# Kernel tuning notes

Hardware: AMD Instinct MI355X
Metric: run time of the kernel (lower is better)

The kernel has to match this reference:

```python
import jax, jax.numpy as jnp
import numpy as np

N = 100000   # nodes
E = 1600000  # edges
IN, H, C = 128, 128, 64
LN_EPS = 1e-5


def _xavier(key, fan_in, fan_out):
    lim = jnp.sqrt(6.0 / (fan_in + fan_out)).astype(jnp.float32)
    return jax.random.uniform(key, (fan_in, fan_out), jnp.float32, -lim, lim)


def setup_inputs() -> dict:
    key = jax.random.key(0)
    ks = jax.random.split(key, 6)
    feats = jax.random.normal(ks[0], (N, IN), jnp.float32)
    src = jax.random.randint(ks[1], (E,), 0, N, jnp.int32)
    dst = jax.random.randint(ks[2], (E,), 0, N, jnp.int32)
    return {
        "feats": feats, "src": src, "dst": dst,
        "W0": _xavier(ks[3], IN, H), "b0": jnp.zeros((H,), jnp.float32),
        "g0": jnp.ones((H,), jnp.float32), "be0": jnp.zeros((H,), jnp.float32),
        "W1": _xavier(ks[4], H, H), "b1": jnp.zeros((H,), jnp.float32),
        "g1": jnp.ones((H,), jnp.float32), "be1": jnp.zeros((H,), jnp.float32),
        "W2": _xavier(ks[5], H, C), "b2": jnp.zeros((C,), jnp.float32),
    }


def _gcn_agg(h, src, dst):
    # symmetric GCN normalization: out[v] = sum_{(u,v) in E} h[u] / sqrt(deg_out(u) * deg_in(v))
    ones = jnp.ones(src.shape, jnp.float32)
    deg_out = jax.ops.segment_sum(ones, src, num_segments=N)
    deg_in = jax.ops.segment_sum(ones, dst, num_segments=N)
    norm_o = jax.lax.rsqrt(jnp.maximum(deg_out, 1.0))
    norm_i = jax.lax.rsqrt(jnp.maximum(deg_in, 1.0))
    msg = (h * norm_o[:, None])[src]                       # [E, d] gather
    agg = jax.ops.segment_sum(msg, dst, num_segments=N)    # [N, d] scatter-add
    return agg * norm_i[:, None]


def _layernorm(x, gamma, beta):
    mu = jnp.mean(x, axis=-1, keepdims=True)
    var = jnp.mean(jnp.square(x - mu), axis=-1, keepdims=True)
    return (x - mu) * jax.lax.rsqrt(var + LN_EPS) * gamma + beta


def reference(feats, src, dst, W0, b0, g0, be0, W1, b1, g1, be1, W2, b2):
    # layer 0: agg -> matmul -> bias -> dropout(eval: identity) -> layernorm -> relu
    h = _gcn_agg(feats, src, dst) @ W0 + b0
    h = jax.nn.relu(_layernorm(h, g0, be0))
    # layer 1
    h = _gcn_agg(h, src, dst) @ W1 + b1
    h = jax.nn.relu(_layernorm(h, g1, be1))
    # final layer: agg -> matmul -> bias
    out = _gcn_agg(h, src, dst) @ W2 + b2
    return out
```

## Files before the change

### kernel.cpp

```cpp
#include <hip/hip_runtime.h>

constexpr float LN_EPS = 1e-5f;

typedef __bf16 bf16x8 __attribute__((ext_vector_type(8)));
typedef float f32x4 __attribute__((ext_vector_type(4)));

__device__ __forceinline__ unsigned short f2bf(float f) {
  unsigned int u = __float_as_uint(f);
  u = (u + 0x7fffu + ((u >> 16) & 1u)) >> 16;
  return (unsigned short)u;
}
__device__ __forceinline__ unsigned int pk2(float x, float y) {
  return (unsigned int)f2bf(x) | ((unsigned int)f2bf(y) << 16);
}
__device__ __forceinline__ float bflo(unsigned int p) { return __uint_as_float(p << 16); }
__device__ __forceinline__ float bfhi(unsigned int p) { return __uint_as_float(p & 0xffff0000u); }

#define NPB 256
#define CHUNK 4096

__global__ __launch_bounds__(256) void passA_kernel(
    const int* __restrict__ src, const int* __restrict__ dst,
    int* __restrict__ cntD, int* __restrict__ cntS, int NB, int NBLK, int E) {
  extern __shared__ int sh[];
  for (int j = threadIdx.x; j < 2 * NB; j += 256) sh[j] = 0;
  __syncthreads();
  const int blk = blockIdx.x;
  const int base = blk * CHUNK;
  const int end = min(base + CHUNK, E);
  for (int i = base + threadIdx.x; i < end; i += 256) {
    atomicAdd(&sh[dst[i] >> 8], 1);
    atomicAdd(&sh[NB + (src[i] >> 8)], 1);
  }
  __syncthreads();
  for (int j = threadIdx.x; j < NB; j += 256) {
    cntD[j * NBLK + blk] = sh[j];
    cntS[j * NBLK + blk] = sh[NB + j];
  }
}

__global__ __launch_bounds__(512) void scan1_kernel(
    const int* __restrict__ cntD, const int* __restrict__ cntS,
    int* __restrict__ offLD, int* __restrict__ offLS,
    int* __restrict__ totD, int* __restrict__ totS, int NB, int NBLK) {
  __shared__ int p[512];
  const int t = threadIdx.x;
  const bool isS = blockIdx.x >= NB;
  const int b = isS ? blockIdx.x - NB : blockIdx.x;
  const int* cnt = isS ? cntS : cntD;
  int* offL = isS ? offLS : offLD;
  int own = (t < NBLK) ? cnt[b * NBLK + t] : 0;
  p[t] = own;
  __syncthreads();
  for (int off = 1; off < 512; off <<= 1) {
    int x = (t >= off) ? p[t - off] : 0;
    __syncthreads();
    p[t] += x;
    __syncthreads();
  }
  if (t < NBLK) offL[b * NBLK + t] = p[t] - own;
  if (t == 511) (isS ? totS : totD)[b] = p[511];
}

__global__ __launch_bounds__(512) void scan2_kernel(
    const int* __restrict__ totD, const int* __restrict__ totS,
    int* __restrict__ bktD, int* __restrict__ bktS,
    int* __restrict__ row_st, int NB, int N, int E) {
  __shared__ int p[512];
  const int t = threadIdx.x;
  int own = (t < NB) ? totD[t] : 0;
  p[t] = own;
  __syncthreads();
  for (int off = 1; off < 512; off <<= 1) {
    int x = (t >= off) ? p[t - off] : 0;
    __syncthreads();
    p[t] += x;
    __syncthreads();
  }
  if (t < NB) bktD[t] = p[t] - own;
  __syncthreads();
  int own2 = (t < NB) ? totS[t] : 0;
  p[t] = own2;
  __syncthreads();
  for (int off = 1; off < 512; off <<= 1) {
    int x = (t >= off) ? p[t - off] : 0;
    __syncthreads();
    p[t] += x;
    __syncthreads();
  }
  if (t < NB) bktS[t] = p[t] - own2;
  if (t == 0) {
    bktD[NB] = E;
    bktS[NB] = E;
    row_st[N] = E;
  }
}

__global__ __launch_bounds__(256) void passB_kernel(
    const int* __restrict__ src, const int* __restrict__ dst,
    const int* __restrict__ offLD, const int* __restrict__ offLS,
    const int* __restrict__ bkt_stD, const int* __restrict__ bkt_stS,
    unsigned int* __restrict__ packedD, unsigned char* __restrict__ srcS,
    int NB, int NBLK, int E) {
  __shared__ unsigned int sD[CHUNK];
  __shared__ unsigned short bD_[CHUNK];
  __shared__ unsigned char sS_[CHUNK];
  __shared__ unsigned short bS_[CHUNK];
  __shared__ int hD[512], lD[512], hS[512], lS[512];
  const int t = threadIdx.x;
  const int blk = blockIdx.x;
  const int base = blk * CHUNK;
  const int end = min(base + CHUNK, E);
  const int cnt = end - base;
  hD[t] = 0; hD[t + 256] = 0; hS[t] = 0; hS[t + 256] = 0;
  __syncthreads();
  for (int i = base + t; i < end; i += 256) {
    atomicAdd(&hD[dst[i] >> 8], 1);
    atomicAdd(&hS[src[i] >> 8], 1);
  }
  __syncthreads();
  int oD0 = hD[t], oD1 = hD[t + 256], oS0 = hS[t], oS1 = hS[t + 256];
  for (int off = 1; off < 512; off <<= 1) {
    int xd0 = (t >= off) ? hD[t - off] : 0;
    int xd1 = (t + 256 >= off) ? hD[t + 256 - off] : 0;
    int xs0 = (t >= off) ? hS[t - off] : 0;
    int xs1 = (t + 256 >= off) ? hS[t + 256 - off] : 0;
    __syncthreads();
    hD[t] += xd0; hD[t + 256] += xd1;
    hS[t] += xs0; hS[t + 256] += xs1;
    __syncthreads();
  }
  lD[t] = hD[t] - oD0; lD[t + 256] = hD[t + 256] - oD1;
  lS[t] = hS[t] - oS0; lS[t + 256] = hS[t + 256] - oS1;
  __syncthreads();
  hD[t] = lD[t]; hD[t + 256] = lD[t + 256];
  hS[t] = lS[t]; hS[t + 256] = lS[t + 256];
  __syncthreads();
  for (int i = base + t; i < end; i += 256) {
    const int d = dst[i];
    const int s = src[i];
    const int bD = d >> 8;
    const int pD = atomicAdd(&hD[bD], 1);
    sD[pD] = ((unsigned int)(d & 255) << 24) | (unsigned int)s;
    bD_[pD] = (unsigned short)bD;
    const int bS = s >> 8;
    const int pS = atomicAdd(&hS[bS], 1);
    sS_[pS] = (unsigned char)(s & 255);
    bS_[pS] = (unsigned short)bS;
  }
  __syncthreads();
  for (int i = t; i < cnt; i += 256) {
    const int bD = bD_[i];
    packedD[bkt_stD[bD] + offLD[bD * NBLK + blk] + (i - lD[bD])] = sD[i];
    const int bS = bS_[i];
    srcS[bkt_stS[bS] + offLS[bS * NBLK + blk] + (i - lS[bS])] = sS_[i];
  }
}

__global__ __launch_bounds__(256) void passC_kernel(
    const unsigned int* __restrict__ packed, const int* __restrict__ bucket_start,
    int* __restrict__ row_st, float* __restrict__ ni,
    int* __restrict__ edge_src, int N) {
  __shared__ int cnt[NPB];
  __shared__ int cur[NPB];
  __shared__ int tmp[NPB];
  const int b = blockIdx.x;
  const int t = threadIdx.x;
  const int v0 = b * NPB;
  const int bs = bucket_start[b];
  const int be = bucket_start[b + 1];
  cnt[t] = 0;
  __syncthreads();
  for (int i = bs + t; i < be; i += 256)
    atomicAdd(&cnt[packed[i] >> 24], 1);
  __syncthreads();
  int own = cnt[t];
  tmp[t] = own;
  __syncthreads();
  for (int off = 1; off < NPB; off <<= 1) {
    int x = (t >= off) ? tmp[t - off] : 0;
    __syncthreads();
    tmp[t] += x;
    __syncthreads();
  }
  const int pref = tmp[t] - own;
  if (v0 + t < N) {
    row_st[v0 + t] = bs + pref;
    ni[v0 + t] = rsqrtf(fmaxf((float)own, 1.0f));
  }
  cur[t] = bs + pref;
  __syncthreads();
  for (int i = bs + t; i < be; i += 256) {
    unsigned int p = packed[i];
    int pos = atomicAdd(&cur[p >> 24], 1);
    edge_src[pos] = (int)(p & 0xFFFFFFu);
  }
}

__global__ __launch_bounds__(256) void passD_kernel(
    const unsigned char* __restrict__ srcS, const int* __restrict__ bkt_stS,
    float* __restrict__ no, int N) {
  __shared__ int cnt[NPB];
  const int b = blockIdx.x;
  const int t = threadIdx.x;
  cnt[t] = 0;
  __syncthreads();
  const int bs = bkt_stS[b];
  const int be = bkt_stS[b + 1];
  for (int i = bs + t; i < be; i += 256)
    atomicAdd(&cnt[srcS[i]], 1);
  __syncthreads();
  const int v = b * NPB + t;
  if (v < N) no[v] = rsqrtf(fmaxf((float)cnt[t], 1.0f));
}

__global__ void wconv_kernel(const float* __restrict__ W, unsigned short* __restrict__ Wt,
                             int K, int C) {
  int i = blockIdx.x * blockDim.x + threadIdx.x;
  if (i < K * C) {
    int k = i / C, c = i - k * C;
    Wt[c * K + k] = f2bf(W[i]);
  }
}

__global__ __launch_bounds__(256) void featconv_kernel(const float* __restrict__ F,
                                                       const float* __restrict__ no,
                                                       unsigned short* __restrict__ out, int N) {
  int row = blockIdx.x * 8 + (threadIdx.x >> 5);
  if (row >= N) return;
  int c = (threadIdx.x & 31) * 4;
  float4 v = *reinterpret_cast<const float4*>(F + (size_t)row * 128 + c);
  float nof = no[row];
  uint2 p = {pk2(v.x * nof, v.y * nof), pk2(v.z * nof, v.w * nof)};
  *reinterpret_cast<uint2*>(out + (size_t)row * 128 + c) = p;
}

__global__ __launch_bounds__(256) void gather_agg_b(
    const unsigned short* __restrict__ hB, const int* __restrict__ row_start,
    const int* __restrict__ edge_src, const float* __restrict__ ni,
    unsigned short* __restrict__ aggB, int N) {
  const int v = blockIdx.x * 4 + (threadIdx.x >> 6);
  if (v >= N) return;
  const int l = threadIdx.x & 63;
  const int half = l >> 5;
  const int lane = l & 31;
  const int s = row_start[v];
  const int e = row_start[v + 1];
  const int co = 4 * lane;
  float a0 = 0, a1 = 0, a2 = 0, a3 = 0;
  float b0 = 0, b1 = 0, b2 = 0, b3 = 0;
  float c0 = 0, c1 = 0, c2 = 0, c3 = 0;
  float d0 = 0, d1 = 0, d2 = 0, d3 = 0;
  int j = s;
  for (; j + 8 <= e; j += 8) {
    int u0 = edge_src[j + half];
    int u1 = edge_src[j + 2 + half];
    int u2 = edge_src[j + 4 + half];
    int u3 = edge_src[j + 6 + half];
    uint2 p0 = *reinterpret_cast<const uint2*>(hB + (size_t)u0 * 128 + co);
    uint2 p1 = *reinterpret_cast<const uint2*>(hB + (size_t)u1 * 128 + co);
    uint2 p2 = *reinterpret_cast<const uint2*>(hB + (size_t)u2 * 128 + co);
    uint2 p3 = *reinterpret_cast<const uint2*>(hB + (size_t)u3 * 128 + co);
    a0 += bflo(p0.x); a1 += bfhi(p0.x); a2 += bflo(p0.y); a3 += bfhi(p0.y);
    b0 += bflo(p1.x); b1 += bfhi(p1.x); b2 += bflo(p1.y); b3 += bfhi(p1.y);
    c0 += bflo(p2.x); c1 += bfhi(p2.x); c2 += bflo(p2.y); c3 += bfhi(p2.y);
    d0 += bflo(p3.x); d1 += bfhi(p3.x); d2 += bflo(p3.y); d3 += bfhi(p3.y);
  }
  for (; j + 2 <= e; j += 2) {
    int u0 = edge_src[j + half];
    uint2 p0 = *reinterpret_cast<const uint2*>(hB + (size_t)u0 * 128 + co);
    a0 += bflo(p0.x); a1 += bfhi(p0.x); a2 += bflo(p0.y); a3 += bfhi(p0.y);
  }
  if (j < e && half == 0) {
    int u0 = edge_src[j];
    uint2 p0 = *reinterpret_cast<const uint2*>(hB + (size_t)u0 * 128 + co);
    a0 += bflo(p0.x); a1 += bfhi(p0.x); a2 += bflo(p0.y); a3 += bfhi(p0.y);
  }
  a0 = (a0 + b0) + (c0 + d0);
  a1 = (a1 + b1) + (c1 + d1);
  a2 = (a2 + b2) + (c2 + d2);
  a3 = (a3 + b3) + (c3 + d3);
  a0 += __shfl_xor(a0, 32);
  a1 += __shfl_xor(a1, 32);
  a2 += __shfl_xor(a2, 32);
  a3 += __shfl_xor(a3, 32);
  if (half == 0) {
    const float niv = ni[v];
    uint2 po = {pk2(a0 * niv, a1 * niv), pk2(a2 * niv, a3 * niv)};
    *reinterpret_cast<uint2*>(aggB + (size_t)v * 128 + co) = po;
  }
}

__global__ __launch_bounds__(256) void gather_out(
    const unsigned short* __restrict__ zB, const int* __restrict__ row_start,
    const int* __restrict__ edge_src, const float* __restrict__ ni,
    const float* __restrict__ bias, float* __restrict__ out, int N) {
  const int v = blockIdx.x * 4 + (threadIdx.x >> 6);
  if (v >= N) return;
  const int l = threadIdx.x & 63;
  const int half = l >> 5;
  const int lane = l & 31;
  const int s = row_start[v];
  const int e = row_start[v + 1];
  const int co = 2 * lane;
  float a0 = 0, a1 = 0, b0 = 0, b1 = 0, c0 = 0, c1 = 0, d0 = 0, d1 = 0;
  int j = s;
  for (; j + 8 <= e; j += 8) {
    int u0 = edge_src[j + half];
    int u1 = edge_src[j + 2 + half];
    int u2 = edge_src[j + 4 + half];
    int u3 = edge_src[j + 6 + half];
    unsigned int p0 = *reinterpret_cast<const unsigned int*>(zB + (size_t)u0 * 64 + co);
    unsigned int p1 = *reinterpret_cast<const unsigned int*>(zB + (size_t)u1 * 64 + co);
    unsigned int p2 = *reinterpret_cast<const unsigned int*>(zB + (size_t)u2 * 64 + co);
    unsigned int p3 = *reinterpret_cast<const unsigned int*>(zB + (size_t)u3 * 64 + co);
    a0 += bflo(p0); a1 += bfhi(p0);
    b0 += bflo(p1); b1 += bfhi(p1);
    c0 += bflo(p2); c1 += bfhi(p2);
    d0 += bflo(p3); d1 += bfhi(p3);
  }
  for (; j + 2 <= e; j += 2) {
    int u0 = edge_src[j + half];
    unsigned int p0 = *reinterpret_cast<const unsigned int*>(zB + (size_t)u0 * 64 + co);
    a0 += bflo(p0); a1 += bfhi(p0);
  }
  if (j < e && half == 0) {
    int u0 = edge_src[j];
    unsigned int p0 = *reinterpret_cast<const unsigned int*>(zB + (size_t)u0 * 64 + co);
    a0 += bflo(p0); a1 += bfhi(p0);
  }
  a0 = (a0 + b0) + (c0 + d0);
  a1 = (a1 + b1) + (c1 + d1);
  a0 += __shfl_xor(a0, 32);
  a1 += __shfl_xor(a1, 32);
  if (half == 0) {
    const float niv = ni[v];
    float2 bb = *reinterpret_cast<const float2*>(bias + co);
    float2 w = {a0 * niv + bb.x, a1 * niv + bb.y};
    *reinterpret_cast<float2*>(out + (size_t)v * 64 + co) = w;
  }
}

__global__ __launch_bounds__(256) void mm_mfma_ln(
    const unsigned short* __restrict__ A, const unsigned short* __restrict__ Wt,
    const float* __restrict__ b, const float* __restrict__ g,
    const float* __restrict__ be, const float* __restrict__ no,
    unsigned short* __restrict__ out, int N) {
  __shared__ float sS[2][2][16];
  __shared__ float sQ[2][2][16];
  __shared__ float sNo[32];
  const int rbase = blockIdx.x * 32;
  const int w = threadIdx.x >> 6;
  const int l = threadIdx.x & 63;
  const int rt = w & 1, ch = w >> 1;
  if (threadIdx.x < 32) sNo[threadIdx.x] = no[min(rbase + (int)threadIdx.x, N - 1)];
  const int arow = min(rbase + rt * 16 + (l & 15), N - 1);
  const int kof = (l >> 4) * 8;

  bf16x8 af[4];
  const unsigned short* ap = A + (size_t)arow * 128 + kof;
#pragma unroll
  for (int kk = 0; kk < 4; ++kk)
    af[kk] = *reinterpret_cast<const bf16x8*>(ap + kk * 32);

  f32x4 acc[4] = {};
#pragma unroll
  for (int ct = 0; ct < 4; ++ct) {
    const int ccol = ch * 64 + ct * 16 + (l & 15);
    const unsigned short* bp = Wt + (size_t)ccol * 128 + kof;
#pragma unroll
    for (int kk = 0; kk < 4; ++kk) {
      bf16x8 bfr = *reinterpret_cast<const bf16x8*>(bp + kk * 32);
      acc[ct] = __builtin_amdgcn_mfma_f32_16x16x32_bf16(af[kk], bfr, acc[ct], 0, 0, 0);
    }
  }

  float s[4] = {0.f, 0.f, 0.f, 0.f}, q[4] = {0.f, 0.f, 0.f, 0.f};
#pragma unroll
  for (int ct = 0; ct < 4; ++ct) {
    const float bc = b[ch * 64 + ct * 16 + (l & 15)];
#pragma unroll
    for (int j = 0; j < 4; ++j) {
      float v = acc[ct][j] + bc;
      acc[ct][j] = v;
      s[j] += v;
      q[j] += v * v;
    }
  }
#pragma unroll
  for (int j = 0; j < 4; ++j) {
#pragma unroll
    for (int off = 1; off < 16; off <<= 1) {
      s[j] += __shfl_xor(s[j], off);
      q[j] += __shfl_xor(q[j], off);
    }
  }
  const int grp = l >> 4;
  if ((l & 15) == 0) {
#pragma unroll
    for (int j = 0; j < 4; ++j) {
      sS[rt][ch][grp * 4 + j] = s[j];
      sQ[rt][ch][grp * 4 + j] = q[j];
    }
  }
  __syncthreads();

#pragma unroll
  for (int j = 0; j < 4; ++j) {
    const int r = grp * 4 + j;
    const int row = rbase + rt * 16 + r;
    float S = sS[rt][0][r] + sS[rt][1][r];
    float Q = sQ[rt][0][r] + sQ[rt][1][r];
    float mu = S * (1.f / 128.f);
    float rstd = rsqrtf(fmaxf(Q * (1.f / 128.f) - mu * mu, 0.f) + LN_EPS);
    float nof = sNo[rt * 16 + r];
    if (row < N) {
#pragma unroll
      for (int ct = 0; ct < 4; ++ct) {
        const int ccol = ch * 64 + ct * 16 + (l & 15);
        float y = (acc[ct][j] - mu) * rstd * g[ccol] + be[ccol];
        y = fmaxf(y, 0.f) * nof;
        out[(size_t)row * 128 + ccol] = f2bf(y);
      }
    }
  }
}

__global__ __launch_bounds__(256) void mm_z_mfma(
    const unsigned short* __restrict__ A, const unsigned short* __restrict__ Wt,
    unsigned short* __restrict__ zB, int N) {
  const int rbase = blockIdx.x * 32;
  const int w = threadIdx.x >> 6;
  const int l = threadIdx.x & 63;
  const int rt = w & 1, ch = w >> 1;
  const int arow = min(rbase + rt * 16 + (l & 15), N - 1);
  const int kof = (l >> 4) * 8;

  bf16x8 af[4];
  const unsigned short* ap = A + (size_t)arow * 128 + kof;
#pragma unroll
  for (int kk = 0; kk < 4; ++kk)
    af[kk] = *reinterpret_cast<const bf16x8*>(ap + kk * 32);

  f32x4 acc[2] = {};
#pragma unroll
  for (int ct = 0; ct < 2; ++ct) {
    const int ccol = ch * 32 + ct * 16 + (l & 15);
    const unsigned short* bp = Wt + (size_t)ccol * 128 + kof;
#pragma unroll
    for (int kk = 0; kk < 4; ++kk) {
      bf16x8 bfr = *reinterpret_cast<const bf16x8*>(bp + kk * 32);
      acc[ct] = __builtin_amdgcn_mfma_f32_16x16x32_bf16(af[kk], bfr, acc[ct], 0, 0, 0);
    }
  }
  const int grp = l >> 4;
#pragma unroll
  for (int ct = 0; ct < 2; ++ct) {
    const int ccol = ch * 32 + ct * 16 + (l & 15);
#pragma unroll
    for (int j = 0; j < 4; ++j) {
      const int row = rbase + rt * 16 + grp * 4 + j;
      if (row < N) zB[(size_t)row * 64 + ccol] = f2bf(acc[ct][j]);
    }
  }
}

extern "C" void kernel_launch(void* const* d_in, const int* in_sizes, int n_in,
                              void* d_out, int out_size, void* d_ws, size_t ws_size,
                              hipStream_t stream) {
  const float* feats = (const float*)d_in[0];
  const int*   src   = (const int*)d_in[1];
  const int*   dst   = (const int*)d_in[2];
  const float* W0    = (const float*)d_in[3];
  const float* b0    = (const float*)d_in[4];
  const float* g0    = (const float*)d_in[5];
  const float* be0   = (const float*)d_in[6];
  const float* W1    = (const float*)d_in[7];
  const float* b1    = (const float*)d_in[8];
  const float* g1    = (const float*)d_in[9];
  const float* be1   = (const float*)d_in[10];
  const float* W2    = (const float*)d_in[11];
  const float* b2    = (const float*)d_in[12];
  float* out = (float*)d_out;

  const int n = in_sizes[0] / 128;
  const int e = in_sizes[1];
  const int NB = (n + NPB - 1) / NPB;
  const int NBLK = (e + CHUNK - 1) / CHUNK;

  float* ws = (float*)d_ws;
  auto pad4 = [](size_t x) { return (x + 3) & ~(size_t)3; };
  size_t o = 0;
  float* norm_o  = ws + o; o = pad4(o + n);
  float* norm_i  = ws + o; o = pad4(o + n);
  int*   cntD    = (int*)(ws + o); o = pad4(o + (size_t)NB * NBLK);
  int*   cntS    = (int*)(ws + o); o = pad4(o + (size_t)NB * NBLK);
  int*   offLD   = (int*)(ws + o); o = pad4(o + (size_t)NB * NBLK);
  int*   offLS   = (int*)(ws + o); o = pad4(o + (size_t)NB * NBLK);
  int*   totD    = (int*)(ws + o); o = pad4(o + NB);
  int*   totS    = (int*)(ws + o); o = pad4(o + NB);
  int*   bkt_stD = (int*)(ws + o); o = pad4(o + NB + 1);
  int*   bkt_stS = (int*)(ws + o); o = pad4(o + NB + 1);
  int*   row_st  = (int*)(ws + o); o = pad4(o + n + 1);
  unsigned int*  packedD = (unsigned int*)(ws + o);  o = pad4(o + (size_t)e);
  unsigned char* srcS    = (unsigned char*)(ws + o); o = pad4(o + (size_t)(e + 3) / 4);
  int*   edg_src = (int*)(ws + o); o = pad4(o + (size_t)e);
  unsigned short* featB = (unsigned short*)(ws + o); o = pad4(o + (size_t)n * 64);
  unsigned short* aggB  = (unsigned short*)(ws + o); o = pad4(o + (size_t)n * 64);
  unsigned short* Wt0   = (unsigned short*)(ws + o); o = pad4(o + 128 * 128 / 2);
  unsigned short* Wt1   = (unsigned short*)(ws + o); o = pad4(o + 128 * 128 / 2);
  unsigned short* Wt2   = (unsigned short*)(ws + o); o = pad4(o + 128 * 64 / 2);
  unsigned short* hB = featB;
  unsigned short* zB = aggB;

  passA_kernel<<<NBLK, 256, 2 * NB * sizeof(int), stream>>>(src, dst, cntD, cntS, NB, NBLK, e);
  scan1_kernel<<<2 * NB, 512, 0, stream>>>(cntD, cntS, offLD, offLS, totD, totS, NB, NBLK);
  scan2_kernel<<<1, 512, 0, stream>>>(totD, totS, bkt_stD, bkt_stS, row_st, NB, n, e);
  passB_kernel<<<NBLK, 256, 0, stream>>>(src, dst, offLD, offLS, bkt_stD, bkt_stS,
                                         packedD, srcS, NB, NBLK, e);
  passC_kernel<<<NB, 256, 0, stream>>>(packedD, bkt_stD, row_st, norm_i, edg_src, n);
  passD_kernel<<<NB, 256, 0, stream>>>(srcS, bkt_stS, norm_o, n);

  wconv_kernel<<<(128 * 128 + 255) / 256, 256, 0, stream>>>(W0, Wt0, 128, 128);
  wconv_kernel<<<(128 * 128 + 255) / 256, 256, 0, stream>>>(W1, Wt1, 128, 128);
  wconv_kernel<<<(128 * 64 + 255) / 256, 256, 0, stream>>>(W2, Wt2, 128, 64);
  featconv_kernel<<<(n + 7) / 8, 256, 0, stream>>>(feats, norm_o, featB, n);

  const int gblocks = (n + 3) / 4;
  const int mblocks = (n + 31) / 32;

  gather_agg_b<<<gblocks, 256, 0, stream>>>(featB, row_st, edg_src, norm_i, aggB, n);
  mm_mfma_ln<<<mblocks, 256, 0, stream>>>(aggB, Wt0, b0, g0, be0, norm_o, hB, n);
  gather_agg_b<<<gblocks, 256, 0, stream>>>(hB, row_st, edg_src, norm_i, aggB, n);
  mm_mfma_ln<<<mblocks, 256, 0, stream>>>(aggB, Wt1, b1, g1, be1, norm_o, hB, n);
  mm_z_mfma<<<mblocks, 256, 0, stream>>>(hB, Wt2, zB, n);
  gather_out<<<gblocks, 256, 0, stream>>>(zB, row_st, edg_src, norm_i, b2, out, n);
}
```

Measured before the change: 397.3 us.

## Switch activations to fp16 with packed half2 accumulation and vectorize CSR build passes

Activations and weights are now stored as fp16 instead of bf16, the gather kernels accumulate with packed __hadd2, and the matmuls use the f16 MFMA intrinsic. The CSR build passes read edges as int4/uint4 vectors, and passB reuses the per-block histograms from passA instead of recounting them. The aim is fewer ALU instructions in the gather loops and less redundant memory traffic during preprocessing. Accumulating in fp16 raises the risk of precision loss or overflow on high-degree nodes.

```diff
diff --git a/kernel.cpp b/kernel.cpp
--- a/kernel.cpp
+++ b/kernel.cpp
@@ -1,20 +1,20 @@
 #include <hip/hip_runtime.h>
+#include <hip/hip_fp16.h>
 
 constexpr float LN_EPS = 1e-5f;
 
-typedef __bf16 bf16x8 __attribute__((ext_vector_type(8)));
+typedef _Float16 f16x8 __attribute__((ext_vector_type(8)));
 typedef float f32x4 __attribute__((ext_vector_type(4)));
 
-__device__ __forceinline__ unsigned short f2bf(float f) {
-  unsigned int u = __float_as_uint(f);
-  u = (u + 0x7fffu + ((u >> 16) & 1u)) >> 16;
-  return (unsigned short)u;
-}
-__device__ __forceinline__ unsigned int pk2(float x, float y) {
-  return (unsigned int)f2bf(x) | ((unsigned int)f2bf(y) << 16);
-}
-__device__ __forceinline__ float bflo(unsigned int p) { return __uint_as_float(p << 16); }
-__device__ __forceinline__ float bfhi(unsigned int p) { return __uint_as_float(p & 0xffff0000u); }
+__device__ __forceinline__ unsigned short f2h(float f) {
+  return __half_as_ushort(__float2half_rn(f));
+}
+__device__ __forceinline__ unsigned int pk2h(float x, float y) {
+  return (unsigned int)f2h(x) | ((unsigned int)f2h(y) << 16);
+}
+__device__ __forceinline__ __half2 u2h2(unsigned int u) {
+  return *reinterpret_cast<__half2*>(&u);
+}
 
 #define NPB 256
 #define CHUNK 4096
@@ -28,9 +28,21 @@
   const int blk = blockIdx.x;
   const int base = blk * CHUNK;
   const int end = min(base + CHUNK, E);
-  for (int i = base + threadIdx.x; i < end; i += 256) {
-    atomicAdd(&sh[dst[i] >> 8], 1);
-    atomicAdd(&sh[NB + (src[i] >> 8)], 1);
+  const int cnt = end - base;
+  const int nv = cnt >> 2;
+  const int4* d4p = reinterpret_cast<const int4*>(dst + base);
+  const int4* s4p = reinterpret_cast<const int4*>(src + base);
+  for (int q = threadIdx.x; q < nv; q += 256) {
+    int4 d4 = d4p[q];
+    int4 s4 = s4p[q];
+    atomicAdd(&sh[d4.x >> 8], 1); atomicAdd(&sh[d4.y >> 8], 1);
+    atomicAdd(&sh[d4.z >> 8], 1); atomicAdd(&sh[d4.w >> 8], 1);
+    atomicAdd(&sh[NB + (s4.x >> 8)], 1); atomicAdd(&sh[NB + (s4.y >> 8)], 1);
+    atomicAdd(&sh[NB + (s4.z >> 8)], 1); atomicAdd(&sh[NB + (s4.w >> 8)], 1);
+  }
+  for (int i = (nv << 2) + threadIdx.x; i < cnt; i += 256) {
+    atomicAdd(&sh[dst[base + i] >> 8], 1);
+    atomicAdd(&sh[NB + (src[base + i] >> 8)], 1);
   }
   __syncthreads();
   for (int j = threadIdx.x; j < NB; j += 256) {
@@ -98,6 +110,7 @@
 
 __global__ __launch_bounds__(256) void passB_kernel(
     const int* __restrict__ src, const int* __restrict__ dst,
+    const int* __restrict__ cntD, const int* __restrict__ cntS,
     const int* __restrict__ offLD, const int* __restrict__ offLS,
     const int* __restrict__ bkt_stD, const int* __restrict__ bkt_stS,
     unsigned int* __restrict__ packedD, unsigned char* __restrict__ srcS,
@@ -112,12 +125,10 @@
   const int base = blk * CHUNK;
   const int end = min(base + CHUNK, E);
   const int cnt = end - base;
-  hD[t] = 0; hD[t + 256] = 0; hS[t] = 0; hS[t + 256] = 0;
-  __syncthreads();
-  for (int i = base + t; i < end; i += 256) {
-    atomicAdd(&hD[dst[i] >> 8], 1);
-    atomicAdd(&hS[src[i] >> 8], 1);
-  }
+  hD[t] = (t < NB) ? cntD[t * NBLK + blk] : 0;
+  hD[t + 256] = (t + 256 < NB) ? cntD[(t + 256) * NBLK + blk] : 0;
+  hS[t] = (t < NB) ? cntS[t * NBLK + blk] : 0;
+  hS[t + 256] = (t + 256 < NB) ? cntS[(t + 256) * NBLK + blk] : 0;
   __syncthreads();
   int oD0 = hD[t], oD1 = hD[t + 256], oS0 = hS[t], oS1 = hS[t + 256];
   for (int off = 1; off < 512; off <<= 1) {
@@ -136,9 +147,29 @@
   hD[t] = lD[t]; hD[t + 256] = lD[t + 256];
   hS[t] = lS[t]; hS[t + 256] = lS[t + 256];
   __syncthreads();
-  for (int i = base + t; i < end; i += 256) {
-    const int d = dst[i];
-    const int s = src[i];
+  const int nv = cnt >> 2;
+  const int4* d4p = reinterpret_cast<const int4*>(dst + base);
+  const int4* s4p = reinterpret_cast<const int4*>(src + base);
+  for (int q = t; q < nv; q += 256) {
+    int4 d4 = d4p[q];
+    int4 s4 = s4p[q];
+#pragma unroll
+    for (int k = 0; k < 4; ++k) {
+      const int d = (&d4.x)[k];
+      const int s = (&s4.x)[k];
+      const int bD = d >> 8;
+      const int pD = atomicAdd(&hD[bD], 1);
+      sD[pD] = ((unsigned int)(d & 255) << 24) | (unsigned int)s;
+      bD_[pD] = (unsigned short)bD;
+      const int bS = s >> 8;
+      const int pS = atomicAdd(&hS[bS], 1);
+      sS_[pS] = (unsigned char)(s & 255);
+      bS_[pS] = (unsigned short)bS;
+    }
+  }
+  for (int i = (nv << 2) + t; i < cnt; i += 256) {
+    const int d = dst[base + i];
+    const int s = src[base + i];
     const int bD = d >> 8;
     const int pD = atomicAdd(&hD[bD], 1);
     sD[pD] = ((unsigned int)(d & 255) << 24) | (unsigned int)s;
@@ -171,7 +202,18 @@
   const int be = bucket_start[b + 1];
   cnt[t] = 0;
   __syncthreads();
-  for (int i = bs + t; i < be; i += 256)
+  const int a0 = bs + ((4 - (bs & 3)) & 3);
+  const int a1 = a0 + (((be - a0) >> 2) << 2);
+  for (int i = bs + t; i < min(a0, be); i += 256)
+    atomicAdd(&cnt[packed[i] >> 24], 1);
+  const uint4* p4 = reinterpret_cast<const uint4*>(packed + a0);
+  const int nv = (a1 - a0) >> 2;
+  for (int q = t; q < nv; q += 256) {
+    uint4 p = p4[q];
+    atomicAdd(&cnt[p.x >> 24], 1); atomicAdd(&cnt[p.y >> 24], 1);
+    atomicAdd(&cnt[p.z >> 24], 1); atomicAdd(&cnt[p.w >> 24], 1);
+  }
+  for (int i = max(a1, bs) + t; i < be; i += 256)
     atomicAdd(&cnt[packed[i] >> 24], 1);
   __syncthreads();
   int own = cnt[t];
@@ -190,7 +232,21 @@
   }
   cur[t] = bs + pref;
   __syncthreads();
-  for (int i = bs + t; i < be; i += 256) {
+  for (int i = bs + t; i < min(a0, be); i += 256) {
+    unsigned int p = packed[i];
+    int pos = atomicAdd(&cur[p >> 24], 1);
+    edge_src[pos] = (int)(p & 0xFFFFFFu);
+  }
+  for (int q = t; q < nv; q += 256) {
+    uint4 p = p4[q];
+#pragma unroll
+    for (int k = 0; k < 4; ++k) {
+      unsigned int pv = (&p.x)[k];
+      int pos = atomicAdd(&cur[pv >> 24], 1);
+      edge_src[pos] = (int)(pv & 0xFFFFFFu);
+    }
+  }
+  for (int i = max(a1, bs) + t; i < be; i += 256) {
     unsigned int p = packed[i];
     int pos = atomicAdd(&cur[p >> 24], 1);
     edge_src[pos] = (int)(p & 0xFFFFFFu);
@@ -219,7 +275,7 @@
   int i = blockIdx.x * blockDim.x + threadIdx.x;
   if (i < K * C) {
     int k = i / C, c = i - k * C;
-    Wt[c * K + k] = f2bf(W[i]);
+    Wt[c * K + k] = f2h(W[i]);
   }
 }
 
@@ -231,14 +287,14 @@
   int c = (threadIdx.x & 31) * 4;
   float4 v = *reinterpret_cast<const float4*>(F + (size_t)row * 128 + c);
   float nof = no[row];
-  uint2 p = {pk2(v.x * nof, v.y * nof), pk2(v.z * nof, v.w * nof)};
+  uint2 p = {pk2h(v.x * nof, v.y * nof), pk2h(v.z * nof, v.w * nof)};
   *reinterpret_cast<uint2*>(out + (size_t)row * 128 + c) = p;
 }
 
-__global__ __launch_bounds__(256) void gather_agg_b(
-    const unsigned short* __restrict__ hB, const int* __restrict__ row_start,
+__global__ __launch_bounds__(256) void gather_agg_h(
+    const unsigned short* __restrict__ hH, const int* __restrict__ row_start,
     const int* __restrict__ edge_src, const float* __restrict__ ni,
-    unsigned short* __restrict__ aggB, int N) {
+    unsigned short* __restrict__ aggH, int N) {
   const int v = blockIdx.x * 4 + (threadIdx.x >> 6);
   if (v >= N) return;
   const int l = threadIdx.x & 63;
@@ -247,52 +303,50 @@
   const int s = row_start[v];
   const int e = row_start[v + 1];
   const int co = 4 * lane;
-  float a0 = 0, a1 = 0, a2 = 0, a3 = 0;
-  float b0 = 0, b1 = 0, b2 = 0, b3 = 0;
-  float c0 = 0, c1 = 0, c2 = 0, c3 = 0;
-  float d0 = 0, d1 = 0, d2 = 0, d3 = 0;
+  const __half2 z = __float2half2_rn(0.f);
+  __half2 A0 = z, A1 = z, B0 = z, B1 = z, C0 = z, C1 = z, D0 = z, D1 = z;
   int j = s;
   for (; j + 8 <= e; j += 8) {
     int u0 = edge_src[j + half];
     int u1 = edge_src[j + 2 + half];
     int u2 = edge_src[j + 4 + half];
     int u3 = edge_src[j + 6 + half];
-    uint2 p0 = *reinterpret_cast<const uint2*>(hB + (size_t)u0 * 128 + co);
-    uint2 p1 = *reinterpret_cast<const uint2*>(hB + (size_t)u1 * 128 + co);
-    uint2 p2 = *reinterpret_cast<const uint2*>(hB + (size_t)u2 * 128 + co);
-    uint2 p3 = *reinterpret_cast<const uint2*>(hB + (size_t)u3 * 128 + co);
-    a0 += bflo(p0.x); a1 += bfhi(p0.x); a2 += bflo(p0.y); a3 += bfhi(p0.y);
-    b0 += bflo(p1.x); b1 += bfhi(p1.x); b2 += bflo(p1.y); b3 += bfhi(p1.y);
-    c0 += bflo(p2.x); c1 += bfhi(p2.x); c2 += bflo(p2.y); c3 += bfhi(p2.y);
-    d0 += bflo(p3.x); d1 += bfhi(p3.x); d2 += bflo(p3.y); d3 += bfhi(p3.y);
+    uint2 p0 = *reinterpret_cast<const uint2*>(hH + (size_t)u0 * 128 + co);
+    uint2 p1 = *reinterpret_cast<const uint2*>(hH + (size_t)u1 * 128 + co);
+    uint2 p2 = *reinterpret_cast<const uint2*>(hH + (size_t)u2 * 128 + co);
+    uint2 p3 = *reinterpret_cast<const uint2*>(hH + (size_t)u3 * 128 + co);
+    A0 = __hadd2(A0, u2h2(p0.x)); A1 = __hadd2(A1, u2h2(p0.y));
+    B0 = __hadd2(B0, u2h2(p1.x)); B1 = __hadd2(B1, u2h2(p1.y));
+    C0 = __hadd2(C0, u2h2(p2.x)); C1 = __hadd2(C1, u2h2(p2.y));
+    D0 = __hadd2(D0, u2h2(p3.x)); D1 = __hadd2(D1, u2h2(p3.y));
   }
   for (; j + 2 <= e; j += 2) {
     int u0 = edge_src[j + half];
-    uint2 p0 = *reinterpret_cast<const uint2*>(hB + (size_t)u0 * 128 + co);
-    a0 += bflo(p0.x); a1 += bfhi(p0.x); a2 += bflo(p0.y); a3 += bfhi(p0.y);
+    uint2 p0 = *reinterpret_cast<const uint2*>(hH + (size_t)u0 * 128 + co);
+    A0 = __hadd2(A0, u2h2(p0.x)); A1 = __hadd2(A1, u2h2(p0.y));
   }
   if (j < e && half == 0) {
     int u0 = edge_src[j];
-    uint2 p0 = *reinterpret_cast<const uint2*>(hB + (size_t)u0 * 128 + co);
-    a0 += bflo(p0.x); a1 += bfhi(p0.x); a2 += bflo(p0.y); a3 += bfhi(p0.y);
-  }
-  a0 = (a0 + b0) + (c0 + d0);
-  a1 = (a1 + b1) + (c1 + d1);
-  a2 = (a2 + b2) + (c2 + d2);
-  a3 = (a3 + b3) + (c3 + d3);
+    uint2 p0 = *reinterpret_cast<const uint2*>(hH + (size_t)u0 * 128 + co);
+    A0 = __hadd2(A0, u2h2(p0.x)); A1 = __hadd2(A1, u2h2(p0.y));
+  }
+  float a0 = (__low2float(A0) + __low2float(B0)) + (__low2float(C0) + __low2float(D0));
+  float a1 = (__high2float(A0) + __high2float(B0)) + (__high2float(C0) + __high2float(D0));
+  float a2 = (__low2float(A1) + __low2float(B1)) + (__low2float(C1) + __low2float(D1));
+  float a3 = (__high2float(A1) + __high2float(B1)) + (__high2float(C1) + __high2float(D1));
   a0 += __shfl_xor(a0, 32);
   a1 += __shfl_xor(a1, 32);
   a2 += __shfl_xor(a2, 32);
   a3 += __shfl_xor(a3, 32);
   if (half == 0) {
     const float niv = ni[v];
-    uint2 po = {pk2(a0 * niv, a1 * niv), pk2(a2 * niv, a3 * niv)};
-    *reinterpret_cast<uint2*>(aggB + (size_t)v * 128 + co) = po;
+    uint2 po = {pk2h(a0 * niv, a1 * niv), pk2h(a2 * niv, a3 * niv)};
+    *reinterpret_cast<uint2*>(aggH + (size_t)v * 128 + co) = po;
   }
 }
 
 __global__ __launch_bounds__(256) void gather_out(
-    const unsigned short* __restrict__ zB, const int* __restrict__ row_start,
+    const unsigned short* __restrict__ zH, const int* __restrict__ row_start,
     const int* __restrict__ edge_src, const float* __restrict__ ni,
     const float* __restrict__ bias, float* __restrict__ out, int N) {
   const int v = blockIdx.x * 4 + (threadIdx.x >> 6);
@@ -303,34 +357,29 @@
   const int s = row_start[v];
   const int e = row_start[v + 1];
   const int co = 2 * lane;
-  float a0 = 0, a1 = 0, b0 = 0, b1 = 0, c0 = 0, c1 = 0, d0 = 0, d1 = 0;
+  const __half2 z = __float2half2_rn(0.f);
+  __half2 A = z, B = z, C = z, D = z;
   int j = s;
   for (; j + 8 <= e; j += 8) {
     int u0 = edge_src[j + half];
     int u1 = edge_src[j + 2 + half];
     int u2 = edge_src[j + 4 + half];
     int u3 = edge_src[j + 6 + half];
-    unsigned int p0 = *reinterpret_cast<const unsigned int*>(zB + (size_t)u0 * 64 + co);
-    unsigned int p1 = *reinterpret_cast<const unsigned int*>(zB + (size_t)u1 * 64 + co);
-    unsigned int p2 = *reinterpret_cast<const unsigned int*>(zB + (size_t)u2 * 64 + co);
-    unsigned int p3 = *reinterpret_cast<const unsigned int*>(zB + (size_t)u3 * 64 + co);
-    a0 += bflo(p0); a1 += bfhi(p0);
-    b0 += bflo(p1); b1 += bfhi(p1);
-    c0 += bflo(p2); c1 += bfhi(p2);
-    d0 += bflo(p3); d1 += bfhi(p3);
+    A = __hadd2(A, u2h2(*reinterpret_cast<const unsigned int*>(zH + (size_t)u0 * 64 + co)));
+    B = __hadd2(B, u2h2(*reinterpret_cast<const unsigned int*>(zH + (size_t)u1 * 64 + co)));
+    C = __hadd2(C, u2h2(*reinterpret_cast<const unsigned int*>(zH + (size_t)u2 * 64 + co)));
+    D = __hadd2(D, u2h2(*reinterpret_cast<const unsigned int*>(zH + (size_t)u3 * 64 + co)));
   }
   for (; j + 2 <= e; j += 2) {
     int u0 = edge_src[j + half];
-    unsigned int p0 = *reinterpret_cast<const unsigned int*>(zB + (size_t)u0 * 64 + co);
-    a0 += bflo(p0); a1 += bfhi(p0);
+    A = __hadd2(A, u2h2(*reinterpret_cast<const unsigned int*>(zH + (size_t)u0 * 64 + co)));
   }
   if (j < e && half == 0) {
     int u0 = edge_src[j];
-    unsigned int p0 = *reinterpret_cast<const unsigned int*>(zB + (size_t)u0 * 64 + co);
-    a0 += bflo(p0); a1 += bfhi(p0);
-  }
-  a0 = (a0 + b0) + (c0 + d0);
-  a1 = (a1 + b1) + (c1 + d1);
+    A = __hadd2(A, u2h2(*reinterpret_cast<const unsigned int*>(zH + (size_t)u0 * 64 + co)));
+  }
+  float a0 = (__low2float(A) + __low2float(B)) + (__low2float(C) + __low2float(D));
+  float a1 = (__high2float(A) + __high2float(B)) + (__high2float(C) + __high2float(D));
   a0 += __shfl_xor(a0, 32);
   a1 += __shfl_xor(a1, 32);
   if (half == 0) {
@@ -357,11 +406,11 @@
   const int arow = min(rbase + rt * 16 + (l & 15), N - 1);
   const int kof = (l >> 4) * 8;
 
-  bf16x8 af[4];
+  f16x8 af[4];
   const unsigned short* ap = A + (size_t)arow * 128 + kof;
 #pragma unroll
   for (int kk = 0; kk < 4; ++kk)
-    af[kk] = *reinterpret_cast<const bf16x8*>(ap + kk * 32);
+    af[kk] = *reinterpret_cast<const f16x8*>(ap + kk * 32);
 
   f32x4 acc[4] = {};
 #pragma unroll
@@ -370,8 +419,8 @@
     const unsigned short* bp = Wt + (size_t)ccol * 128 + kof;
 #pragma unroll
     for (int kk = 0; kk < 4; ++kk) {
-      bf16x8 bfr = *reinterpret_cast<const bf16x8*>(bp + kk * 32);
-      acc[ct] = __builtin_amdgcn_mfma_f32_16x16x32_bf16(af[kk], bfr, acc[ct], 0, 0, 0);
+      f16x8 bfr = *reinterpret_cast<const f16x8*>(bp + kk * 32);
+      acc[ct] = __builtin_amdgcn_mfma_f32_16x16x32_f16(af[kk], bfr, acc[ct], 0, 0, 0);
     }
   }
 
@@ -420,7 +469,7 @@
         const int ccol = ch * 64 + ct * 16 + (l & 15);
         float y = (acc[ct][j] - mu) * rstd * g[ccol] + be[ccol];
         y = fmaxf(y, 0.f) * nof;
-        out[(size_t)row * 128 + ccol] = f2bf(y);
+        out[(size_t)row * 128 + ccol] = f2h(y);
       }
     }
   }
@@ -428,7 +477,7 @@
 
 __global__ __launch_bounds__(256) void mm_z_mfma(
     const unsigned short* __restrict__ A, const unsigned short* __restrict__ Wt,
-    unsigned short* __restrict__ zB, int N) {
+    unsigned short* __restrict__ zH, int N) {
   const int rbase = blockIdx.x * 32;
   const int w = threadIdx.x >> 6;
   const int l = threadIdx.x & 63;
@@ -436,11 +485,11 @@
   const int arow = min(rbase + rt * 16 + (l & 15), N - 1);
   const int kof = (l >> 4) * 8;
 
-  bf16x8 af[4];
+  f16x8 af[4];
   const unsigned short* ap = A + (size_t)arow * 128 + kof;
 #pragma unroll
   for (int kk = 0; kk < 4; ++kk)
-    af[kk] = *reinterpret_cast<const bf16x8*>(ap + kk * 32);
+    af[kk] = *reinterpret_cast<const f16x8*>(ap + kk * 32);
 
   f32x4 acc[2] = {};
 #pragma unroll
@@ -449,8 +498,8 @@
     const unsigned short* bp = Wt + (size_t)ccol * 128 + kof;
 #pragma unroll
     for (int kk = 0; kk < 4; ++kk) {
-      bf16x8 bfr = *reinterpret_cast<const bf16x8*>(bp + kk * 32);
-      acc[ct] = __builtin_amdgcn_mfma_f32_16x16x32_bf16(af[kk], bfr, acc[ct], 0, 0, 0);
+      f16x8 bfr = *reinterpret_cast<const f16x8*>(bp + kk * 32);
+      acc[ct] = __builtin_amdgcn_mfma_f32_16x16x32_f16(af[kk], bfr, acc[ct], 0, 0, 0);
     }
   }
   const int grp = l >> 4;
@@ -460,7 +509,7 @@
 #pragma unroll
     for (int j = 0; j < 4; ++j) {
       const int row = rbase + rt * 16 + grp * 4 + j;
-      if (row < N) zB[(size_t)row * 64 + ccol] = f2bf(acc[ct][j]);
+      if (row < N) zH[(size_t)row * 64 + ccol] = f2h(acc[ct][j]);
     }
   }
 }
@@ -505,18 +554,18 @@
   unsigned int*  packedD = (unsigned int*)(ws + o);  o = pad4(o + (size_t)e);
   unsigned char* srcS    = (unsigned char*)(ws + o); o = pad4(o + (size_t)(e + 3) / 4);
   int*   edg_src = (int*)(ws + o); o = pad4(o + (size_t)e);
-  unsigned short* featB = (unsigned short*)(ws + o); o = pad4(o + (size_t)n * 64);
-  unsigned short* aggB  = (unsigned short*)(ws + o); o = pad4(o + (size_t)n * 64);
+  unsigned short* featH = (unsigned short*)(ws + o); o = pad4(o + (size_t)n * 64);
+  unsigned short* aggH  = (unsigned short*)(ws + o); o = pad4(o + (size_t)n * 64);
   unsigned short* Wt0   = (unsigned short*)(ws + o); o = pad4(o + 128 * 128 / 2);
   unsigned short* Wt1   = (unsigned short*)(ws + o); o = pad4(o + 128 * 128 / 2);
   unsigned short* Wt2   = (unsigned short*)(ws + o); o = pad4(o + 128 * 64 / 2);
-  unsigned short* hB = featB;
-  unsigned short* zB = aggB;
+  unsigned short* hH = featH;
+  unsigned short* zH = aggH;
 
   passA_kernel<<<NBLK, 256, 2 * NB * sizeof(int), stream>>>(src, dst, cntD, cntS, NB, NBLK, e);
   scan1_kernel<<<2 * NB, 512, 0, stream>>>(cntD, cntS, offLD, offLS, totD, totS, NB, NBLK);
   scan2_kernel<<<1, 512, 0, stream>>>(totD, totS, bkt_stD, bkt_stS, row_st, NB, n, e);
-  passB_kernel<<<NBLK, 256, 0, stream>>>(src, dst, offLD, offLS, bkt_stD, bkt_stS,
+  passB_kernel<<<NBLK, 256, 0, stream>>>(src, dst, cntD, cntS, offLD, offLS, bkt_stD, bkt_stS,
                                          packedD, srcS, NB, NBLK, e);
   passC_kernel<<<NB, 256, 0, stream>>>(packedD, bkt_stD, row_st, norm_i, edg_src, n);
   passD_kernel<<<NB, 256, 0, stream>>>(srcS, bkt_stS, norm_o, n);
@@ -524,15 +573,15 @@
   wconv_kernel<<<(128 * 128 + 255) / 256, 256, 0, stream>>>(W0, Wt0, 128, 128);
   wconv_kernel<<<(128 * 128 + 255) / 256, 256, 0, stream>>>(W1, Wt1, 128, 128);
   wconv_kernel<<<(128 * 64 + 255) / 256, 256, 0, stream>>>(W2, Wt2, 128, 64);
-  featconv_kernel<<<(n + 7) / 8, 256, 0, stream>>>(feats, norm_o, featB, n);
+  featconv_kernel<<<(n + 7) / 8, 256, 0, stream>>>(feats, norm_o, featH, n);
 
   const int gblocks = (n + 3) / 4;
   const int mblocks = (n + 31) / 32;
 
-  gather_agg_b<<<gblocks, 256, 0, stream>>>(featB, row_st, edg_src, norm_i, aggB, n);
-  mm_mfma_ln<<<mblocks, 256, 0, stream>>>(aggB, Wt0, b0, g0, be0, norm_o, hB, n);
-  gather_agg_b<<<gblocks, 256, 0, stream>>>(hB, row_st, edg_src, norm_i, aggB, n);
-  mm_mfma_ln<<<mblocks, 256, 0, stream>>>(aggB, Wt1, b1, g1, be1, norm_o, hB, n);
-  mm_z_mfma<<<mblocks, 256, 0, stream>>>(hB, Wt2, zB, n);
-  gather_out<<<gblocks, 256, 0, stream>>>(zB, row_st, edg_src, norm_i, b2, out, n);
-}
+  gather_agg_h<<<gblocks, 256, 0, stream>>>(featH, row_st, edg_src, norm_i, aggH, n);
+  mm_mfma_ln<<<mblocks, 256, 0, stream>>>(aggH, Wt0, b0, g0, be0, norm_o, hH, n);
+  gather_agg_h<<<gblocks, 256, 0, stream>>>(hH, row_st, edg_src, norm_i, aggH, n);
+  mm_mfma_ln<<<mblocks, 256, 0, stream>>>(aggH, Wt1, b1, g1, be1, norm_o, hH, n);
+  mm_z_mfma<<<mblocks, 256, 0, stream>>>(hH, Wt2, zH, n);
+  gather_out<<<gblocks, 256, 0, stream>>>(zH, row_st, edg_src, norm_i, b2, out, n);
+}
```

After: 388.9 us. 1.02x faster.
